# Kernel optimization log

Hardware: AMD Instinct MI355X
Metric: run time of the kernel (lower is better)

The kernel has to match this reference:

```python
import jax, jax.numpy as jnp
import numpy as np

NUM_HEADS = 8
DIMS = 512
SR = 2
EPS = 1e-6


def setup_inputs() -> dict:
    key = jax.random.key(0)
    ks = jax.random.split(key, 12)
    B, H, W, C = 4, 64, 64, DIMS
    s = 0.02
    return {
        "x": jax.random.normal(ks[0], (B, H * W, C), dtype=jnp.float32),
        "Wq": jax.random.normal(ks[1], (C, DIMS), dtype=jnp.float32) * s,
        "bq": jnp.zeros((DIMS,), jnp.float32),
        "Wk": jax.random.normal(ks[2], (C, DIMS), dtype=jnp.float32) * s,
        "bk": jnp.zeros((DIMS,), jnp.float32),
        "Wv": jax.random.normal(ks[3], (C, DIMS), dtype=jnp.float32) * s,
        "bv": jnp.zeros((DIMS,), jnp.float32),
        "Wp": jax.random.normal(ks[4], (DIMS, DIMS), dtype=jnp.float32) * s,
        "bp": jnp.zeros((DIMS,), jnp.float32),
        "sr_w": jax.random.normal(ks[5], (SR, SR, C, DIMS), dtype=jnp.float32) * s,  # HWIO
        "sr_b": jnp.zeros((DIMS,), jnp.float32),
        "ln_g": jnp.ones((DIMS,), jnp.float32),
        "ln_b": jnp.zeros((DIMS,), jnp.float32),
        "H": 64,
        "W": 64,
    }


def reference(x, Wq, bq, Wk, bk, Wv, bv, Wp, bp, sr_w, sr_b, ln_g, ln_b, H, W):
    B, N, C = x.shape
    hd = DIMS // NUM_HEADS

    # spatial-reduction of K/V: strided conv (kernel=stride=SR, SAME) + LayerNorm
    kv = x.reshape(B, H, W, C)
    kv = jax.lax.conv_general_dilated(
        kv, sr_w, window_strides=(SR, SR), padding="SAME",
        dimension_numbers=("NHWC", "HWIO", "NHWC")) + sr_b
    kv = kv.reshape(B, -1, C)  # [B, Nk, C], Nk = (H//SR)*(W//SR)
    mu = jnp.mean(kv, axis=-1, keepdims=True)
    var = jnp.mean(jnp.square(kv - mu), axis=-1, keepdims=True)
    kv = (kv - mu) * jax.lax.rsqrt(var + EPS) * ln_g + ln_b
    Nk = kv.shape[1]

    # NOTE: original splits heads as reshape(B, N, head_dims, num_heads) and
    # indexes the LAST axis per head -> head h sees channels d*NUM_HEADS+h.
    q = (x @ Wq + bq).reshape(B, N, hd, NUM_HEADS)
    k = (kv @ Wk + bk).reshape(B, Nk, hd, NUM_HEADS)
    v = (kv @ Wv + bv).reshape(B, Nk, hd, NUM_HEADS)

    scores = jnp.einsum("bqdh,bkdh->bhqk", q, k) / jnp.sqrt(jnp.float32(hd))
    w = jax.nn.softmax(scores, axis=-1)
    # concat of heads along channels -> (B, N, NUM_HEADS, hd) layout
    out = jnp.einsum("bhqk,bkdh->bqhd", w, v).reshape(B, N, DIMS)
    return out @ Wp + bp
```

## Files before the change

### kernel.cpp

```cpp
#include <hip/hip_runtime.h>


typedef __attribute__((ext_vector_type(8))) _Float16 f16x8;
typedef __attribute__((ext_vector_type(4))) _Float16 f16x4;
typedef __attribute__((ext_vector_type(4))) float f32x4;

#define EXP2F(x) __builtin_amdgcn_exp2f(x)

__device__ __forceinline__ void gload_lds16(const _Float16* g, _Float16* l)
{
    __builtin_amdgcn_global_load_lds(
        (const __attribute__((address_space(1))) void*)g,
        (__attribute__((address_space(3))) void*)l, 16, 0, 0);
}

__global__ __launch_bounds__(256)
void cvt_x_k(const float* __restrict__ in, _Float16* __restrict__ out)
{
    const size_t i = ((size_t)blockIdx.x * 256 + threadIdx.x) * 8;
    const float4 a = *(const float4*)(in + i);
    const float4 b = *(const float4*)(in + i + 4);
    f16x8 o;
    o[0] = (_Float16)a.x; o[1] = (_Float16)a.y; o[2] = (_Float16)a.z; o[3] = (_Float16)a.w;
    o[4] = (_Float16)b.x; o[5] = (_Float16)b.y; o[6] = (_Float16)b.z; o[7] = (_Float16)b.w;
    *(f16x8*)(out + i) = o;
}

__global__ __launch_bounds__(256)
void trans4_k(const float* __restrict__ Wq, const float* __restrict__ Wk,
              const float* __restrict__ Wv, const float* __restrict__ Wp,
              _Float16* __restrict__ wqt, _Float16* __restrict__ wkvt,
              _Float16* __restrict__ wpt)
{
    const float* src; _Float16* dst; int perm;
    switch (blockIdx.z) {
        case 0:  src = Wq; dst = wqt;           perm = 1; break;
        case 1:  src = Wk; dst = wkvt;          perm = 1; break;
        case 2:  src = Wv; dst = wkvt + 262144; perm = 0; break;
        default: src = Wp; dst = wpt;           perm = 0; break;
    }
    __shared__ float T[32][33];
    const int n0 = blockIdx.x * 32, k0 = blockIdx.y * 32;
    const int t = threadIdx.x;
    {
        const int r = t >> 3, c = (t & 7) * 4;
        const float4 v = *(const float4*)(src + (size_t)(k0 + r) * 512 + n0 + c);
        T[r][c + 0] = v.x; T[r][c + 1] = v.y; T[r][c + 2] = v.z; T[r][c + 3] = v.w;
    }
    __syncthreads();
    {
        const int j = t >> 3, i0 = (t & 7) * 4;
        const int n = n0 + j;
        const int nper = perm ? ((n & 7) * 64 + (n >> 3)) : n;
        f16x4 o;
        o[0] = (_Float16)T[i0 + 0][j];
        o[1] = (_Float16)T[i0 + 1][j];
        o[2] = (_Float16)T[i0 + 2][j];
        o[3] = (_Float16)T[i0 + 3][j];
        *(f16x4*)(dst + (size_t)nper * 512 + k0 + i0) = o;
    }
}

__global__ __launch_bounds__(256)
void trans_srw_k(const float* __restrict__ in, _Float16* __restrict__ out)
{
    __shared__ float T[32][33];
    const int n0 = blockIdx.x * 32, k0 = blockIdx.y * 32;
    const int t = threadIdx.x;
    {
        const int r = t >> 3, c = (t & 7) * 4;
        const float4 v = *(const float4*)(in + (size_t)(k0 + r) * 512 + n0 + c);
        T[r][c + 0] = v.x; T[r][c + 1] = v.y; T[r][c + 2] = v.z; T[r][c + 3] = v.w;
    }
    __syncthreads();
    {
        const int j = t >> 3, i0 = (t & 7) * 4;
        f16x4 o;
        o[0] = (_Float16)T[i0 + 0][j];
        o[1] = (_Float16)T[i0 + 1][j];
        o[2] = (_Float16)T[i0 + 2][j];
        o[3] = (_Float16)T[i0 + 3][j];
        *(f16x4*)(out + (size_t)(n0 + j) * 2048 + k0 + i0) = o;
    }
}

template<int MODE, bool CONV, int BM>
__global__ __launch_bounds__(256)
void gemm_f16(const _Float16* __restrict__ A, const _Float16* __restrict__ Wt,
              const float* __restrict__ bias, const float* __restrict__ bias2,
              void* __restrict__ Cv, void* __restrict__ Cv2)
{
    constexpr int K = CONV ? 2048 : 512;
    constexpr int MT = BM / 32;
    constexpr int AI = BM / 64;
    __shared__ __align__(16) _Float16 As[BM * 32];
    __shared__ __align__(16) _Float16 Ws[128 * 32];
    const int tid = threadIdx.x;
    const int wave = tid >> 6, lane = tid & 63;
    const int quad = lane >> 4, l15 = lane & 15;
    const int wm = wave >> 1, wn = wave & 1;
    const int wrow = wm * (BM / 2);
    const int m0 = blockIdx.y * BM, n0 = blockIdx.x * 128;

    f32x4 acc[MT][4] = {};

    for (int k0 = 0; k0 < K; k0 += 32) {
        __syncthreads();
        #pragma unroll
        for (int t = 0; t < AI; ++t) {
            const int ii = wave * AI + t;
            const int e = ii * 64 + lane;
            const int row = e >> 2, c8 = (e & 3) * 8;
            const _Float16* gp;
            if (CONV) {
                const int grow = m0 + row;
                const int b = grow >> 10, rem = grow & 1023;
                const int oh = rem >> 5, ow = rem & 31;
                const int gk = k0 + c8;
                const int ky = (gk >> 10) & 1, kx = (gk >> 9) & 1, ci = gk & 511;
                gp = A + ((size_t)((b * 64 + 2 * oh + ky) * 64) + (2 * ow + kx)) * 512 + ci;
            } else {
                gp = A + (size_t)(m0 + row) * K + k0 + c8;
            }
            gload_lds16(gp, &As[ii * 512]);
        }
        #pragma unroll
        for (int t = 0; t < 2; ++t) {
            const int ii = wave * 2 + t;
            const int e = ii * 64 + lane;
            const int row = e >> 2, c8 = (e & 3) * 8;
            gload_lds16(Wt + (size_t)(n0 + row) * K + k0 + c8, &Ws[ii * 512]);
        }
        __syncthreads();

        f16x8 af[MT], bf[4];
        #pragma unroll
        for (int mt = 0; mt < MT; ++mt)
            af[mt] = *(const f16x8*)&As[(wrow + mt * 16 + l15) * 32 + quad * 8];
        #pragma unroll
        for (int nt = 0; nt < 4; ++nt)
            bf[nt] = *(const f16x8*)&Ws[(wn * 64 + nt * 16 + l15) * 32 + quad * 8];
        #pragma unroll
        for (int mt = 0; mt < MT; ++mt)
            #pragma unroll
            for (int nt = 0; nt < 4; ++nt)
                acc[mt][nt] = __builtin_amdgcn_mfma_f32_16x16x32_f16(
                    af[mt], bf[nt], acc[mt][nt], 0, 0, 0);
    }

    #pragma unroll
    for (int nt = 0; nt < 4; ++nt) {
        const int gcol = n0 + wn * 64 + nt * 16 + l15;
        float bv;
        if (MODE == 6) bv = bias[(gcol & 63) * 8 + (gcol >> 6)];
        else if (MODE == 5) bv = (gcol < 512) ? bias[(gcol & 63) * 8 + (gcol >> 6)]
                                              : bias2[gcol - 512];
        else bv = bias[gcol];
        #pragma unroll
        for (int mt = 0; mt < MT; ++mt) {
            const int row0 = m0 + wrow + mt * 16 + quad * 4;
            if (MODE == 0) {
                #pragma unroll
                for (int r = 0; r < 4; ++r)
                    ((float*)Cv)[(size_t)(row0 + r) * 512 + gcol] = acc[mt][nt][r] + bv;
            } else if (MODE == 4 || MODE == 6) {
                #pragma unroll
                for (int r = 0; r < 4; ++r)
                    ((_Float16*)Cv)[(size_t)(row0 + r) * 512 + gcol] =
                        (_Float16)(acc[mt][nt][r] + bv);
            } else {
                if (gcol < 512) {
                    #pragma unroll
                    for (int r = 0; r < 4; ++r)
                        ((_Float16*)Cv)[(size_t)(row0 + r) * 512 + gcol] =
                            (_Float16)(acc[mt][nt][r] + bv);
                } else {
                    const int c = gcol - 512;
                    const int h = c & 7, d = c >> 3;
                    const int b_ = row0 >> 10, jj = row0 & 1023;
                    f16x4 o;
                    #pragma unroll
                    for (int r = 0; r < 4; ++r) o[r] = (_Float16)(acc[mt][nt][r] + bv);
                    *(f16x4*)((_Float16*)Cv2 +
                              ((size_t)(b_ * 8 + h) * 64 + d) * 1024 + jj) = o;
                }
            }
        }
    }
}

__global__ __launch_bounds__(256)
void ln_k(_Float16* __restrict__ buf, const float* __restrict__ g,
          const float* __restrict__ b)
{
    const int row = blockIdx.x;
    _Float16* p = buf + (size_t)row * 512;
    const int tid = threadIdx.x;
    const float vx = (float)p[tid * 2], vy = (float)p[tid * 2 + 1];
    float s = vx + vy, q = vx * vx + vy * vy;
    #pragma unroll
    for (int off = 32; off > 0; off >>= 1) {
        s += __shfl_xor(s, off);
        q += __shfl_xor(q, off);
    }
    __shared__ float ss[4], sq[4], stat[2];
    const int wid = tid >> 6;
    if ((tid & 63) == 0) { ss[wid] = s; sq[wid] = q; }
    __syncthreads();
    if (tid == 0) {
        const float S = ss[0] + ss[1] + ss[2] + ss[3];
        const float Q = sq[0] + sq[1] + sq[2] + sq[3];
        const float mu = S * (1.f / 512.f);
        const float var = fmaxf(Q * (1.f / 512.f) - mu * mu, 0.f);
        stat[0] = mu;
        stat[1] = rsqrtf(var + 1e-6f);
    }
    __syncthreads();
    const float mu = stat[0], rs = stat[1];
    const float2 gg = *(const float2*)(g + tid * 2);
    const float2 bb = *(const float2*)(b + tid * 2);
    p[tid * 2]     = (_Float16)((vx - mu) * rs * gg.x + bb.x);
    p[tid * 2 + 1] = (_Float16)((vy - mu) * rs * gg.y + bb.y);
}

__global__ __launch_bounds__(512)
void attn_mfma_k(const _Float16* __restrict__ qb,
                 const _Float16* __restrict__ kbuf,
                 const _Float16* __restrict__ vbuf,
                 _Float16* __restrict__ out)
{
    const int bh = blockIdx.y;
    const int qt = blockIdx.x;
    const int b = bh >> 3, h = bh & 7;
    const int tid = threadIdx.x;
    const int wave = tid >> 6, lane = tid & 63;
    const int quad = lane >> 4, l15 = lane & 15;

    __shared__ __align__(16) _Float16 Ks[2][64 * 72];
    __shared__ __align__(16) _Float16 Vs[2][64 * 72];

    const int qrow = b * 4096 + qt * 256 + wave * 32 + l15;
    const _Float16* qp = qb + (size_t)qrow * 512 + h * 64 + quad * 8;
    f16x8 qf[2][2];
    qf[0][0] = *(const f16x8*)qp;
    qf[0][1] = *(const f16x8*)(qp + 32);
    qf[1][0] = *(const f16x8*)(qp + 16 * 512);
    qf[1][1] = *(const f16x8*)(qp + 16 * 512 + 32);
    {
        const _Float16 qs = (_Float16)0.18033688f;
        #pragma unroll
        for (int su = 0; su < 2; ++su)
            #pragma unroll
            for (int g = 0; g < 2; ++g)
                #pragma unroll
                for (int i = 0; i < 8; ++i) qf[su][g][i] *= qs;
    }

    const int kr = tid >> 3, kc = (tid & 7) * 8;
    const _Float16* kg = kbuf + (size_t)(b * 1024 + kr) * 512 + h * 64 + kc;
    const _Float16* vg = vbuf + (size_t)(bh * 64 + kr) * 1024 + kc;

    f16x8 krg = *(const f16x8*)kg;
    f16x8 vrg = *(const f16x8*)vg;
    *(f16x8*)&Ks[0][kr * 72 + kc] = krg;
    *(f16x8*)&Vs[0][kr * 72 + kc] = vrg;

    float l_run[2] = {0.f, 0.f};
    f32x4 acc[2][4] = {};

    for (int kt = 0; kt < 16; ++kt) {
        const int cur = kt & 1;
        __syncthreads();
        if (kt < 15) {
            krg = *(const f16x8*)(kg + (size_t)(kt + 1) * 64 * 512);
            vrg = *(const f16x8*)(vg + (kt + 1) * 64);
        }

        f16x4 pa[2][4];
        #pragma unroll
        for (int ct = 0; ct < 4; ++ct) {
            const f16x8 kf0 = *(const f16x8*)&Ks[cur][(ct * 16 + l15) * 72 + quad * 8];
            const f16x8 kf1 = *(const f16x8*)&Ks[cur][(ct * 16 + l15) * 72 + 32 + quad * 8];
            #pragma unroll
            for (int su = 0; su < 2; ++su) {
                f32x4 s = {};
                s = __builtin_amdgcn_mfma_f32_16x16x32_f16(kf0, qf[su][0], s, 0, 0, 0);
                s = __builtin_amdgcn_mfma_f32_16x16x32_f16(kf1, qf[su][1], s, 0, 0, 0);
                const float p0 = EXP2F(s[0]), p1 = EXP2F(s[1]);
                const float p2 = EXP2F(s[2]), p3 = EXP2F(s[3]);
                l_run[su] += (p0 + p1) + (p2 + p3);
                f16x4 t;
                t[0] = (_Float16)p0; t[1] = (_Float16)p1;
                t[2] = (_Float16)p2; t[3] = (_Float16)p3;
                pa[su][ct] = t;
            }
        }

        #pragma unroll
        for (int nt = 0; nt < 4; ++nt) {
            #pragma unroll
            for (int ct = 0; ct < 4; ++ct) {
                const f16x4 vf = *(const f16x4*)&Vs[cur][(nt * 16 + l15) * 72 + ct * 16 + quad * 4];
                acc[0][nt] = __builtin_amdgcn_mfma_f32_16x16x16f16(
                    pa[0][ct], vf, acc[0][nt], 0, 0, 0);
                acc[1][nt] = __builtin_amdgcn_mfma_f32_16x16x16f16(
                    pa[1][ct], vf, acc[1][nt], 0, 0, 0);
            }
        }

        if (kt < 15) {
            *(f16x8*)&Ks[cur ^ 1][kr * 72 + kc] = krg;
            *(f16x8*)&Vs[cur ^ 1][kr * 72 + kc] = vrg;
        }
    }

    #pragma unroll
    for (int su = 0; su < 2; ++su) {
        float ts = l_run[su];
        ts += __shfl_xor(ts, 16);
        ts += __shfl_xor(ts, 32);
        float inv[4];
        #pragma unroll
        for (int r = 0; r < 4; ++r)
            inv[r] = 1.0f / __shfl(ts, quad * 4 + r, 16);
        #pragma unroll
        for (int nt = 0; nt < 4; ++nt)
            #pragma unroll
            for (int r = 0; r < 4; ++r) {
                const int row = qt * 256 + wave * 32 + su * 16 + quad * 4 + r;
                const int col = h * 64 + nt * 16 + l15;
                out[((size_t)b * 4096 + row) * 512 + col] =
                    (_Float16)(acc[su][nt][r] * inv[r]);
            }
    }
}

extern "C" void kernel_launch(void* const* d_in, const int* in_sizes, int n_in,
                              void* d_out, int out_size, void* d_ws, size_t ws_size,
                              hipStream_t stream)
{
    const float* x   = (const float*)d_in[0];
    const float* Wq  = (const float*)d_in[1];
    const float* bq  = (const float*)d_in[2];
    const float* Wk  = (const float*)d_in[3];
    const float* bk  = (const float*)d_in[4];
    const float* Wv  = (const float*)d_in[5];
    const float* bv  = (const float*)d_in[6];
    const float* Wp  = (const float*)d_in[7];
    const float* bp  = (const float*)d_in[8];
    const float* srw = (const float*)d_in[9];
    const float* srb = (const float*)d_in[10];
    const float* lng = (const float*)d_in[11];
    const float* lnb = (const float*)d_in[12];

    _Float16* ws   = (_Float16*)d_ws;
    _Float16* xh   = ws;
    _Float16* atth = xh + 8388608;
    _Float16* kvh  = atth + 8388608;
    _Float16* kh   = kvh + 2097152;
    _Float16* vh   = kh + 2097152;
    _Float16* wqt  = vh + 2097152;
    _Float16* wkvt = wqt + 262144;
    _Float16* wpt  = wkvt + 524288;
    _Float16* srwt = wpt + 262144;
    _Float16* qh   = (_Float16*)d_out;

    cvt_x_k   <<<4096, 256, 0, stream>>>(x, xh);
    trans4_k  <<<dim3(16, 16, 4), 256, 0, stream>>>(Wq, Wk, Wv, Wp, wqt, wkvt, wpt);
    trans_srw_k<<<dim3(16, 64), 256, 0, stream>>>(srw, srwt);
    gemm_f16<4, true, 64><<<dim3(4, 64), 256, 0, stream>>>(
        xh, srwt, srb, nullptr, kvh, nullptr);
    ln_k<<<4096, 256, 0, stream>>>(kvh, lng, lnb);
    gemm_f16<6, false, 128><<<dim3(4, 128), 256, 0, stream>>>(
        xh, wqt, bq, nullptr, qh, nullptr);
    gemm_f16<5, false, 128><<<dim3(8, 32), 256, 0, stream>>>(
        kvh, wkvt, bk, bv, kh, vh);
    attn_mfma_k<<<dim3(16, 32), 512, 0, stream>>>(qh, kh, vh, atth);
    gemm_f16<0, false, 128><<<dim3(4, 128), 256, 0, stream>>>(
        atth, wpt, bp, nullptr, d_out, nullptr);
}
```

Baseline: 247.0 us.

## Merge prep kernels, co-launch conv and Q GEMMs, widen attention query tiles

Folds the x conversion and all weight transposes into one prep launch, and runs the conv (strided SR) GEMM and the Q projection GEMM as one combined launch with block-index dispatch. The KV projection GEMM drops to 64-row tiles for more blocks. The attention kernel now gives each wave 64 query rows instead of 32, so each K/V tile loaded into LDS serves twice as many queries, and it raises wave priority around the PV MFMA loop. The aim is fewer launches, better GPU fill, and more reuse of K/V per tile. The cost is higher register pressure in attention and only half as many attention blocks.

```diff
diff --git a/kernel.cpp b/kernel.cpp
--- a/kernel.cpp
+++ b/kernel.cpp
@@ -15,92 +15,98 @@
 }
 
 __global__ __launch_bounds__(256)
-void cvt_x_k(const float* __restrict__ in, _Float16* __restrict__ out)
-{
-    const size_t i = ((size_t)blockIdx.x * 256 + threadIdx.x) * 8;
-    const float4 a = *(const float4*)(in + i);
-    const float4 b = *(const float4*)(in + i + 4);
-    f16x8 o;
-    o[0] = (_Float16)a.x; o[1] = (_Float16)a.y; o[2] = (_Float16)a.z; o[3] = (_Float16)a.w;
-    o[4] = (_Float16)b.x; o[5] = (_Float16)b.y; o[6] = (_Float16)b.z; o[7] = (_Float16)b.w;
-    *(f16x8*)(out + i) = o;
-}
-
-__global__ __launch_bounds__(256)
-void trans4_k(const float* __restrict__ Wq, const float* __restrict__ Wk,
-              const float* __restrict__ Wv, const float* __restrict__ Wp,
-              _Float16* __restrict__ wqt, _Float16* __restrict__ wkvt,
-              _Float16* __restrict__ wpt)
-{
-    const float* src; _Float16* dst; int perm;
-    switch (blockIdx.z) {
-        case 0:  src = Wq; dst = wqt;           perm = 1; break;
-        case 1:  src = Wk; dst = wkvt;          perm = 1; break;
-        case 2:  src = Wv; dst = wkvt + 262144; perm = 0; break;
-        default: src = Wp; dst = wpt;           perm = 0; break;
-    }
+void prep_k(const float* __restrict__ x,
+            const float* __restrict__ Wq, const float* __restrict__ Wk,
+            const float* __restrict__ Wv, const float* __restrict__ Wp,
+            const float* __restrict__ srw,
+            _Float16* __restrict__ xh, _Float16* __restrict__ wqt,
+            _Float16* __restrict__ wkvt, _Float16* __restrict__ wpt,
+            _Float16* __restrict__ srwt)
+{
     __shared__ float T[32][33];
-    const int n0 = blockIdx.x * 32, k0 = blockIdx.y * 32;
+    const int id = blockIdx.x;
     const int t = threadIdx.x;
+
+    if (id < 4096) {
+        const size_t i = ((size_t)id * 256 + t) * 8;
+        const float4 a = *(const float4*)(x + i);
+        const float4 b = *(const float4*)(x + i + 4);
+        f16x8 o;
+        o[0] = (_Float16)a.x; o[1] = (_Float16)a.y; o[2] = (_Float16)a.z; o[3] = (_Float16)a.w;
+        o[4] = (_Float16)b.x; o[5] = (_Float16)b.y; o[6] = (_Float16)b.z; o[7] = (_Float16)b.w;
+        *(f16x8*)(xh + i) = o;
+        return;
+    }
+
+    if (id < 5120) {
+        const int id2 = id - 4096;
+        const int z = id2 >> 8, k0 = ((id2 >> 4) & 15) * 32, n0 = (id2 & 15) * 32;
+        const float* src; _Float16* dst; int perm;
+        switch (z) {
+            case 0:  src = Wq; dst = wqt;           perm = 1; break;
+            case 1:  src = Wk; dst = wkvt;          perm = 1; break;
+            case 2:  src = Wv; dst = wkvt + 262144; perm = 0; break;
+            default: src = Wp; dst = wpt;           perm = 0; break;
+        }
+        {
+            const int r = t >> 3, c = (t & 7) * 4;
+            const float4 v = *(const float4*)(src + (size_t)(k0 + r) * 512 + n0 + c);
+            T[r][c + 0] = v.x; T[r][c + 1] = v.y; T[r][c + 2] = v.z; T[r][c + 3] = v.w;
+        }
+        __syncthreads();
+        {
+            const int j = t >> 3, i0 = (t & 7) * 4;
+            const int n = n0 + j;
+            const int nper = perm ? ((n & 7) * 64 + (n >> 3)) : n;
+            f16x4 o;
+            o[0] = (_Float16)T[i0 + 0][j];
+            o[1] = (_Float16)T[i0 + 1][j];
+            o[2] = (_Float16)T[i0 + 2][j];
+            o[3] = (_Float16)T[i0 + 3][j];
+            *(f16x4*)(dst + (size_t)nper * 512 + k0 + i0) = o;
+        }
+        return;
+    }
+
     {
-        const int r = t >> 3, c = (t & 7) * 4;
-        const float4 v = *(const float4*)(src + (size_t)(k0 + r) * 512 + n0 + c);
-        T[r][c + 0] = v.x; T[r][c + 1] = v.y; T[r][c + 2] = v.z; T[r][c + 3] = v.w;
-    }
-    __syncthreads();
-    {
-        const int j = t >> 3, i0 = (t & 7) * 4;
-        const int n = n0 + j;
-        const int nper = perm ? ((n & 7) * 64 + (n >> 3)) : n;
-        f16x4 o;
-        o[0] = (_Float16)T[i0 + 0][j];
-        o[1] = (_Float16)T[i0 + 1][j];
-        o[2] = (_Float16)T[i0 + 2][j];
-        o[3] = (_Float16)T[i0 + 3][j];
-        *(f16x4*)(dst + (size_t)nper * 512 + k0 + i0) = o;
-    }
-}
-
-__global__ __launch_bounds__(256)
-void trans_srw_k(const float* __restrict__ in, _Float16* __restrict__ out)
-{
-    __shared__ float T[32][33];
-    const int n0 = blockIdx.x * 32, k0 = blockIdx.y * 32;
-    const int t = threadIdx.x;
-    {
-        const int r = t >> 3, c = (t & 7) * 4;
-        const float4 v = *(const float4*)(in + (size_t)(k0 + r) * 512 + n0 + c);
-        T[r][c + 0] = v.x; T[r][c + 1] = v.y; T[r][c + 2] = v.z; T[r][c + 3] = v.w;
-    }
-    __syncthreads();
-    {
-        const int j = t >> 3, i0 = (t & 7) * 4;
-        f16x4 o;
-        o[0] = (_Float16)T[i0 + 0][j];
-        o[1] = (_Float16)T[i0 + 1][j];
-        o[2] = (_Float16)T[i0 + 2][j];
-        o[3] = (_Float16)T[i0 + 3][j];
-        *(f16x4*)(out + (size_t)(n0 + j) * 2048 + k0 + i0) = o;
+        const int id3 = id - 5120;
+        const int n0 = (id3 & 15) * 32, k0 = (id3 >> 4) * 32;
+        {
+            const int r = t >> 3, c = (t & 7) * 4;
+            const float4 v = *(const float4*)(srw + (size_t)(k0 + r) * 512 + n0 + c);
+            T[r][c + 0] = v.x; T[r][c + 1] = v.y; T[r][c + 2] = v.z; T[r][c + 3] = v.w;
+        }
+        __syncthreads();
+        {
+            const int j = t >> 3, i0 = (t & 7) * 4;
+            f16x4 o;
+            o[0] = (_Float16)T[i0 + 0][j];
+            o[1] = (_Float16)T[i0 + 1][j];
+            o[2] = (_Float16)T[i0 + 2][j];
+            o[3] = (_Float16)T[i0 + 3][j];
+            *(f16x4*)(srwt + (size_t)(n0 + j) * 2048 + k0 + i0) = o;
+        }
+        return;
     }
 }
 
 template<int MODE, bool CONV, int BM>
-__global__ __launch_bounds__(256)
-void gemm_f16(const _Float16* __restrict__ A, const _Float16* __restrict__ Wt,
-              const float* __restrict__ bias, const float* __restrict__ bias2,
-              void* __restrict__ Cv, void* __restrict__ Cv2)
+__device__ __forceinline__ void gemm_body(
+    const int bx, const int by,
+    const _Float16* __restrict__ A, const _Float16* __restrict__ Wt,
+    const float* __restrict__ bias, const float* __restrict__ bias2,
+    void* __restrict__ Cv, void* __restrict__ Cv2,
+    _Float16* __restrict__ As, _Float16* __restrict__ Ws)
 {
     constexpr int K = CONV ? 2048 : 512;
     constexpr int MT = BM / 32;
     constexpr int AI = BM / 64;
-    __shared__ __align__(16) _Float16 As[BM * 32];
-    __shared__ __align__(16) _Float16 Ws[128 * 32];
     const int tid = threadIdx.x;
     const int wave = tid >> 6, lane = tid & 63;
     const int quad = lane >> 4, l15 = lane & 15;
     const int wm = wave >> 1, wn = wave & 1;
     const int wrow = wm * (BM / 2);
-    const int m0 = blockIdx.y * BM, n0 = blockIdx.x * 128;
+    const int m0 = by * BM, n0 = bx * 128;
 
     f32x4 acc[MT][4] = {};
 
@@ -189,6 +195,37 @@
     }
 }
 
+template<int MODE, bool CONV, int BM>
+__global__ __launch_bounds__(256)
+void gemm_f16(const _Float16* __restrict__ A, const _Float16* __restrict__ Wt,
+              const float* __restrict__ bias, const float* __restrict__ bias2,
+              void* __restrict__ Cv, void* __restrict__ Cv2)
+{
+    __shared__ __align__(16) _Float16 As[BM * 32];
+    __shared__ __align__(16) _Float16 Ws[128 * 32];
+    gemm_body<MODE, CONV, BM>(blockIdx.x, blockIdx.y, A, Wt, bias, bias2,
+                              Cv, Cv2, As, Ws);
+}
+
+__global__ __launch_bounds__(256)
+void convq_k(const _Float16* __restrict__ xh, const _Float16* __restrict__ srwt,
+             const float* __restrict__ srb, const _Float16* __restrict__ wqt,
+             const float* __restrict__ bq,
+             _Float16* __restrict__ kvh, _Float16* __restrict__ qh)
+{
+    __shared__ __align__(16) _Float16 As[128 * 32];
+    __shared__ __align__(16) _Float16 Ws[128 * 32];
+    const int id = blockIdx.x;
+    if (id < 512) {
+        gemm_body<6, false, 128>(id & 3, id >> 2, xh, wqt, bq, nullptr,
+                                 qh, nullptr, As, Ws);
+    } else {
+        const int id2 = id - 512;
+        gemm_body<4, true, 64>(id2 & 3, id2 >> 2, xh, srwt, srb, nullptr,
+                               kvh, nullptr, As, Ws);
+    }
+}
+
 __global__ __launch_bounds__(256)
 void ln_k(_Float16* __restrict__ buf, const float* __restrict__ g,
           const float* __restrict__ b)
@@ -239,17 +276,18 @@
     __shared__ __align__(16) _Float16 Ks[2][64 * 72];
     __shared__ __align__(16) _Float16 Vs[2][64 * 72];
 
-    const int qrow = b * 4096 + qt * 256 + wave * 32 + l15;
+    const int qrow = b * 4096 + qt * 512 + wave * 64 + l15;
     const _Float16* qp = qb + (size_t)qrow * 512 + h * 64 + quad * 8;
-    f16x8 qf[2][2];
-    qf[0][0] = *(const f16x8*)qp;
-    qf[0][1] = *(const f16x8*)(qp + 32);
-    qf[1][0] = *(const f16x8*)(qp + 16 * 512);
-    qf[1][1] = *(const f16x8*)(qp + 16 * 512 + 32);
+    f16x8 qf[4][2];
+    #pragma unroll
+    for (int su = 0; su < 4; ++su) {
+        qf[su][0] = *(const f16x8*)(qp + su * 16 * 512);
+        qf[su][1] = *(const f16x8*)(qp + su * 16 * 512 + 32);
+    }
     {
         const _Float16 qs = (_Float16)0.18033688f;
         #pragma unroll
-        for (int su = 0; su < 2; ++su)
+        for (int su = 0; su < 4; ++su)
             #pragma unroll
             for (int g = 0; g < 2; ++g)
                 #pragma unroll
@@ -265,8 +303,8 @@
     *(f16x8*)&Ks[0][kr * 72 + kc] = krg;
     *(f16x8*)&Vs[0][kr * 72 + kc] = vrg;
 
-    float l_run[2] = {0.f, 0.f};
-    f32x4 acc[2][4] = {};
+    float l_run[4] = {0.f, 0.f, 0.f, 0.f};
+    f32x4 acc[4][4] = {};
 
     for (int kt = 0; kt < 16; ++kt) {
         const int cur = kt & 1;
@@ -276,13 +314,13 @@
             vrg = *(const f16x8*)(vg + (kt + 1) * 64);
         }
 
-        f16x4 pa[2][4];
+        f16x4 pa[4][4];
         #pragma unroll
         for (int ct = 0; ct < 4; ++ct) {
             const f16x8 kf0 = *(const f16x8*)&Ks[cur][(ct * 16 + l15) * 72 + quad * 8];
             const f16x8 kf1 = *(const f16x8*)&Ks[cur][(ct * 16 + l15) * 72 + 32 + quad * 8];
             #pragma unroll
-            for (int su = 0; su < 2; ++su) {
+            for (int su = 0; su < 4; ++su) {
                 f32x4 s = {};
                 s = __builtin_amdgcn_mfma_f32_16x16x32_f16(kf0, qf[su][0], s, 0, 0, 0);
                 s = __builtin_amdgcn_mfma_f32_16x16x32_f16(kf1, qf[su][1], s, 0, 0, 0);
@@ -296,17 +334,19 @@
             }
         }
 
+        __builtin_amdgcn_s_setprio(1);
         #pragma unroll
         for (int nt = 0; nt < 4; ++nt) {
             #pragma unroll
             for (int ct = 0; ct < 4; ++ct) {
                 const f16x4 vf = *(const f16x4*)&Vs[cur][(nt * 16 + l15) * 72 + ct * 16 + quad * 4];
-                acc[0][nt] = __builtin_amdgcn_mfma_f32_16x16x16f16(
-                    pa[0][ct], vf, acc[0][nt], 0, 0, 0);
-                acc[1][nt] = __builtin_amdgcn_mfma_f32_16x16x16f16(
-                    pa[1][ct], vf, acc[1][nt], 0, 0, 0);
+                #pragma unroll
+                for (int su = 0; su < 4; ++su)
+                    acc[su][nt] = __builtin_amdgcn_mfma_f32_16x16x16f16(
+                        pa[su][ct], vf, acc[su][nt], 0, 0, 0);
             }
         }
+        __builtin_amdgcn_s_setprio(0);
 
         if (kt < 15) {
             *(f16x8*)&Ks[cur ^ 1][kr * 72 + kc] = krg;
@@ -315,7 +355,7 @@
     }
 
     #pragma unroll
-    for (int su = 0; su < 2; ++su) {
+    for (int su = 0; su < 4; ++su) {
         float ts = l_run[su];
         ts += __shfl_xor(ts, 16);
         ts += __shfl_xor(ts, 32);
@@ -327,7 +367,7 @@
         for (int nt = 0; nt < 4; ++nt)
             #pragma unroll
             for (int r = 0; r < 4; ++r) {
-                const int row = qt * 256 + wave * 32 + su * 16 + quad * 4 + r;
+                const int row = qt * 512 + wave * 64 + su * 16 + quad * 4 + r;
                 const int col = h * 64 + nt * 16 + l15;
                 out[((size_t)b * 4096 + row) * 512 + col] =
                     (_Float16)(acc[su][nt][r] * inv[r]);
@@ -365,17 +405,13 @@
     _Float16* srwt = wpt + 262144;
     _Float16* qh   = (_Float16*)d_out;
 
-    cvt_x_k   <<<4096, 256, 0, stream>>>(x, xh);
-    trans4_k  <<<dim3(16, 16, 4), 256, 0, stream>>>(Wq, Wk, Wv, Wp, wqt, wkvt, wpt);
-    trans_srw_k<<<dim3(16, 64), 256, 0, stream>>>(srw, srwt);
-    gemm_f16<4, true, 64><<<dim3(4, 64), 256, 0, stream>>>(
-        xh, srwt, srb, nullptr, kvh, nullptr);
+    prep_k<<<6144, 256, 0, stream>>>(x, Wq, Wk, Wv, Wp, srw,
+                                     xh, wqt, wkvt, wpt, srwt);
+    convq_k<<<768, 256, 0, stream>>>(xh, srwt, srb, wqt, bq, kvh, qh);
     ln_k<<<4096, 256, 0, stream>>>(kvh, lng, lnb);
-    gemm_f16<6, false, 128><<<dim3(4, 128), 256, 0, stream>>>(
-        xh, wqt, bq, nullptr, qh, nullptr);
-    gemm_f16<5, false, 128><<<dim3(8, 32), 256, 0, stream>>>(
+    gemm_f16<5, false, 64><<<dim3(8, 64), 256, 0, stream>>>(
         kvh, wkvt, bk, bv, kh, vh);
-    attn_mfma_k<<<dim3(16, 32), 512, 0, stream>>>(qh, kh, vh, atth);
+    attn_mfma_k<<<dim3(8, 32), 512, 0, stream>>>(qh, kh, vh, atth);
     gemm_f16<0, false, 128><<<dim3(4, 128), 256, 0, stream>>>(
         atth, wpt, bp, nullptr, d_out, nullptr);
 }
```

Measured after the change: 231.8 us. -6.2%, faster.
